# Kernel optimization log

Measured on AMD Instinct MI355X. Metric: run time of the kernel, lower is better.

## Reference

```python
import jax, jax.numpy as jnp
import numpy as np

B, S, H = 2, 2048, 2048
NH = 16
NOPE, ROPE, VDIM, RANK = 128, 64, 128, 512
QHD = NOPE + ROPE  # 192
MAX_POS, THETA = 4096, 50000.0
EPS = 1e-6


def rms_norm(x, w):
    var = jnp.mean(x.astype(jnp.float32) ** 2, axis=-1, keepdims=True)
    return (x * jax.lax.rsqrt(var + EPS)).astype(x.dtype) * w


def deinterleave(x):
    # view(..., d//2, 2).transpose(-1,-2).reshape(..., d): [x0,x2,...,x1,x3,...]
    return jnp.concatenate([x[..., ::2], x[..., 1::2]], axis=-1)


def rotate_half(x):
    x1, x2 = jnp.split(x, 2, axis=-1)
    return jnp.concatenate([-x2, x1], axis=-1)


def setup_inputs() -> dict:
    key = jax.random.key(0)
    ks = jax.random.split(key, 6)
    hidden_states = jax.random.normal(ks[0], (B, S, H), dtype=jnp.float32)
    attention_mask = jnp.broadcast_to(jnp.tril(jnp.ones((S, S), dtype=bool))[None, None], (B, 1, S, S))
    position_ids = jnp.broadcast_to(jnp.arange(S, dtype=jnp.int32)[None], (B, S))
    inv_freq = 1.0 / (THETA ** (jnp.arange(0, ROPE, 2, dtype=jnp.float32) / ROPE))
    freqs = jnp.arange(MAX_POS, dtype=jnp.float32)[:, None] * inv_freq[None, :]
    emb = jnp.concatenate([freqs, freqs], axis=-1)
    cos_cache, sin_cache = jnp.cos(emb), jnp.sin(emb)
    Wq = jax.random.normal(ks[1], (H, NH * QHD), dtype=jnp.float32) * 0.02
    Wkv_a = jax.random.normal(ks[2], (H, RANK + ROPE), dtype=jnp.float32) * 0.02
    kv_a_ln_w = jnp.ones((RANK,), dtype=jnp.float32)
    Wkv_b = jax.random.normal(ks[3], (NH, NOPE + VDIM, RANK), dtype=jnp.float32) * 0.02
    Wo = jax.random.normal(ks[4], (NH * VDIM, H), dtype=jnp.float32) * 0.02
    return {"hidden_states": hidden_states, "attention_mask": attention_mask, "position_ids": position_ids,
            "cos_cache": cos_cache, "sin_cache": sin_cache, "Wq": Wq, "Wkv_a": Wkv_a,
            "kv_a_ln_w": kv_a_ln_w, "Wkv_b": Wkv_b, "Wo": Wo}


def reference(hidden_states, attention_mask, position_ids, cos_cache, sin_cache, Wq, Wkv_a, kv_a_ln_w, Wkv_b, Wo):
    bsz, q_len, _ = hidden_states.shape
    scale = QHD ** (-0.5)
    # Q projection: [b,s,h*192] -> [b,h,s,192]
    q = (hidden_states @ Wq).reshape(bsz, q_len, NH, QHD).transpose(0, 2, 1, 3)
    q_nope, q_pe = q[..., :NOPE], q[..., NOPE:]
    # compressed KV + shared rope key: [b,s,576]
    ckv_full = hidden_states @ Wkv_a
    compressed_kv, k_pe = ckv_full[..., :RANK], ckv_full[..., RANK:]
    compressed_kv = rms_norm(compressed_kv, kv_a_ln_w)  # [b,s,512]
    # interleaved -> half layout, then standard RoPE
    q_pe = deinterleave(q_pe)                     # [b,h,s,64]
    k_pe = deinterleave(k_pe)                     # [b,s,64]
    cos = cos_cache[position_ids][:, None]        # [b,1,s,64]
    sin = sin_cache[position_ids][:, None]
    q_pe = q_pe * cos + rotate_half(q_pe) * sin
    k_pe = (k_pe[:, None] * cos + rotate_half(k_pe[:, None]) * sin)[:, 0]  # [b,s,64]
    # weight absorption
    q_absorb = Wkv_b[:, :NOPE]    # [h,128,512]
    out_absorb = Wkv_b[:, NOPE:]  # [h,128,512]
    q_nope_c = jnp.einsum('hdc,bhqd->bhqc', q_absorb, q_nope)  # [b,h,s,512]
    scores = (jnp.einsum('bhqd,bkd->bhqk', q_pe, k_pe)
              + jnp.einsum('bhqc,bkc->bhqk', q_nope_c, compressed_kv)) * scale
    scores = jnp.where(attention_mask, scores, jnp.float32(-1e9))
    probs = jax.nn.softmax(scores.astype(jnp.float32), axis=-1).astype(hidden_states.dtype)
    x = jnp.einsum('bhqk,bkc->bhqc', probs, compressed_kv)     # [b,h,s,512]
    attn = jnp.einsum('bhqc,hdc->bhqd', x, out_absorb)         # [b,h,s,128]
    attn = attn.transpose(0, 2, 1, 3).reshape(bsz, q_len, NH * VDIM)
    return attn @ Wo
```

## Files before the change

### kernel.cpp

```cpp
#include <hip/hip_runtime.h>
#include <math.h>

#define B_    2
#define S_    2048
#define H_    2048
#define NH_   16
#define NOPE_ 128
#define ROPE_ 64
#define VDIM_ 128
#define RANK_ 512
#define QHD_  192
#define DTOT_ 576

typedef short short8 __attribute__((ext_vector_type(8)));
typedef float f32x4 __attribute__((ext_vector_type(4)));

__device__ __forceinline__ unsigned short f2bf(float f) {
    unsigned u = __float_as_uint(f);
    u += 0x7fffu + ((u >> 16) & 1u);
    return (unsigned short)(u >> 16);
}
__device__ __forceinline__ float bf2f(unsigned short u) {
    return __uint_as_float((unsigned)u << 16);
}
__device__ __forceinline__ unsigned pack2bf(float a, float b) {
    return (unsigned)f2bf(a) | ((unsigned)f2bf(b) << 16);
}
__device__ __forceinline__ unsigned long long pack4bf(float a, float b, float c, float d) {
    return (unsigned long long)pack2bf(a, b) | ((unsigned long long)pack2bf(c, d) << 32);
}
union i4s8 { int4 i; short8 s; };

typedef __attribute__((address_space(3))) unsigned int lds_u32_t;
typedef __attribute__((address_space(1))) const unsigned int glob_u32_t;
__device__ __forceinline__ void async_copy16(const unsigned short* g, unsigned short* l) {
    __builtin_amdgcn_global_load_lds((glob_u32_t*)g, (lds_u32_t*)l, 16, 0, 0);
}

__global__ __launch_bounds__(256) void cast_bf16(const float* __restrict__ in,
                                                 unsigned short* __restrict__ out)
{
    const size_t i = ((size_t)blockIdx.x * 256 + threadIdx.x) * 4;
    float4 v = *(const float4*)(in + i);
    *(unsigned long long*)(out + i) = pack4bf(v.x, v.y, v.z, v.w);
}

__global__ __launch_bounds__(256) void transpose_w(const float* __restrict__ in,
                                                   unsigned short* __restrict__ out,
                                                   int Rr, int Cc,
                                                   size_t inBatch, size_t outBatch)
{
    __shared__ unsigned short tl[64][72];
    in  += (size_t)blockIdx.z * inBatch;
    out += (size_t)blockIdx.z * outBatch;
    const int t  = threadIdx.x;
    const int r0 = blockIdx.x * 64;
    const int c0 = blockIdx.y * 64;
    const int lr = t >> 4;
    const int lc = (t & 15) * 4;
#pragma unroll
    for (int r = 0; r < 4; ++r) {
        float4 v = *(const float4*)(in + (size_t)(r0 + lr*4 + r) * Cc + c0 + lc);
        tl[lr*4 + r][lc+0] = f2bf(v.x); tl[lr*4 + r][lc+1] = f2bf(v.y);
        tl[lr*4 + r][lc+2] = f2bf(v.z); tl[lr*4 + r][lc+3] = f2bf(v.w);
    }
    __syncthreads();
#pragma unroll
    for (int r = 0; r < 4; ++r) {
        ushort4 v;
        v.x = tl[lc+0][lr*4+r]; v.y = tl[lc+1][lr*4+r];
        v.z = tl[lc+2][lr*4+r]; v.w = tl[lc+3][lr*4+r];
        *(ushort4*)(out + (size_t)(c0 + lr*4 + r) * Rr + r0 + lc) = v;
    }
}

#define BGEMM_BODY(STORE_STMT)                                                     \
    __shared__ unsigned short Al[128*32];                                          \
    __shared__ unsigned short Bl[128*32];                                          \
    const int t = threadIdx.x;                                                     \
    const int wv = t >> 6;                                                         \
    const int lane = t & 63;                                                       \
    const int lq = lane & 15, quad = lane >> 4;                                    \
    const int m0 = by * 128, n0 = bx * 128;                                        \
    const int wrow = (wv >> 1) * 64, wcol = (wv & 1) * 64;                         \
    const int srow = lane >> 2;                                                    \
    const int scol = (lane & 3) * 8;                                               \
    f32x4 acc[4][4] = {};                                                          \
    for (int k0 = 0; k0 < K; k0 += 32) {                                           \
        _Pragma("unroll")                                                          \
        for (int pA = 0; pA < 2; ++pA) {                                           \
            const unsigned short* src =                                            \
                A + (size_t)(m0 + pA*64 + wv*16 + srow) * lda + k0 + scol;         \
            async_copy16(src, &Al[pA*2048 + wv*512]);                              \
        }                                                                          \
        _Pragma("unroll")                                                          \
        for (int pB = 0; pB < 2; ++pB) {                                           \
            int brow = n0 + pB*64 + wv*16 + srow;                                  \
            if (brow > N - 1) brow = N - 1;                                        \
            const unsigned short* src = B + (size_t)brow * ldb + k0 + scol;        \
            async_copy16(src, &Bl[pB*2048 + wv*512]);                              \
        }                                                                          \
        __syncthreads();                                                           \
        short8 af[4], bf[4];                                                       \
        _Pragma("unroll")                                                          \
        for (int i = 0; i < 4; ++i) {                                              \
            af[i] = *(const short8*)&Al[(wrow + i*16 + lq)*32 + quad*8];           \
            bf[i] = *(const short8*)&Bl[(wcol + i*16 + lq)*32 + quad*8];           \
        }                                                                          \
        _Pragma("unroll")                                                          \
        for (int mi = 0; mi < 4; ++mi)                                             \
            _Pragma("unroll")                                                      \
            for (int ni = 0; ni < 4; ++ni)                                         \
                acc[mi][ni] = __builtin_amdgcn_mfma_f32_16x16x32_bf16(             \
                    af[mi], bf[ni], acc[mi][ni], 0, 0, 0);                         \
        __syncthreads();                                                           \
    }                                                                              \
    _Pragma("unroll")                                                              \
    for (int mi = 0; mi < 4; ++mi)                                                 \
        _Pragma("unroll")                                                          \
        for (int ni = 0; ni < 4; ++ni) {                                           \
            int col = n0 + wcol + ni*16 + lq;                                      \
            if (col < N) {                                                         \
                _Pragma("unroll")                                                  \
                for (int r = 0; r < 4; ++r)                                        \
                    STORE_STMT;                                                    \
            }                                                                      \
        }

#define XCD_SWZ(BX, BY)                                                            \
    {                                                                              \
        const int nx = gridDim.x;                                                  \
        const int nwg = nx * gridDim.y;                                            \
        const int wg = BY * nx + BX;                                               \
        const int nw = (wg & 7) * (nwg >> 3) + (wg >> 3);                          \
        BX = nw % nx; BY = nw / nx;                                                \
    }

__global__ __launch_bounds__(256, 2) void bgemm2(const unsigned short* __restrict__ A,
                                                 int lda,
                                                 const unsigned short* __restrict__ B,
                                                 int ldb,
                                                 unsigned short* __restrict__ C,
                                                 int ldc, int K, int N, int qcmode)
{
    int bx = blockIdx.x, by = blockIdx.y;
    if (qcmode == 1) {
        const int z = blockIdx.z;
        A += (size_t)(z >> 4) * S_ * (NH_*QHD_) + (z & 15) * QHD_;
        B += (size_t)(z & 15) * RANK_ * NOPE_;
        C += (size_t)z * S_ * DTOT_;
    } else if (qcmode == 2) {
        const int z = blockIdx.z;
        A += (size_t)(z & 15) * 256 * RANK_ + (size_t)NOPE_ * RANK_;
        B += (size_t)(z >> 4) * S_ * DTOT_;
        C += (size_t)z * VDIM_ * S_;
    } else {
        XCD_SWZ(bx, by);
    }
    BGEMM_BODY(C[(size_t)(m0 + wrow + mi*16 + quad*4 + r) * ldc + col] = f2bf(acc[mi][ni][r]))
}

__global__ __launch_bounds__(256, 2) void bgemm2f(const unsigned short* __restrict__ A,
                                                  int lda,
                                                  const unsigned short* __restrict__ B,
                                                  int ldb,
                                                  float* __restrict__ C,
                                                  int ldc, int K, int N)
{
    int bx = blockIdx.x, by = blockIdx.y;
    XCD_SWZ(bx, by);
    BGEMM_BODY(C[(size_t)(m0 + wrow + mi*16 + quad*4 + r) * ldc + col] = acc[mi][ni][r])
}

__global__ __launch_bounds__(128) void postkv(const unsigned short* __restrict__ ckv_bf,
                                              const float* __restrict__ lnw,
                                              const int*   __restrict__ pos_ids,
                                              const float* __restrict__ cosc,
                                              const float* __restrict__ sinc,
                                              unsigned short* __restrict__ k_cat)
{
    const int row = blockIdx.x;
    const int t   = threadIdx.x;
    const unsigned short* src = ckv_bf + (size_t)row * DTOT_;
    __shared__ float red[128];

    ushort4 v = *(const ushort4*)(src + t * 4);
    float x0 = bf2f(v.x), x1 = bf2f(v.y), x2 = bf2f(v.z), x3 = bf2f(v.w);
    red[t] = x0*x0 + x1*x1 + x2*x2 + x3*x3;
    __syncthreads();
    for (int off = 64; off > 0; off >>= 1) {
        if (t < off) red[t] += red[t + off];
        __syncthreads();
    }
    const float rs = rsqrtf(red[0] / (float)RANK_ + 1e-6f);

    unsigned short* kc = k_cat + (size_t)row * DTOT_;
    *(unsigned long long*)(kc + t*4) =
        pack4bf(x0*rs*lnw[t*4+0], x1*rs*lnw[t*4+1], x2*rs*lnw[t*4+2], x3*rs*lnw[t*4+3]);

    if (t < 32) {
        const int pos = pos_ids[row];
        const float c  = cosc[pos * ROPE_ + t];
        const float sn = sinc[pos * ROPE_ + t];
        const float y0 = bf2f(src[RANK_ + 2*t]);
        const float y1 = bf2f(src[RANK_ + 2*t + 1]);
        kc[RANK_ + t]      = f2bf(y0*c - y1*sn);
        kc[RANK_ + 32 + t] = f2bf(y1*c + y0*sn);
    }
}

__global__ __launch_bounds__(512) void ropeq(const unsigned short* __restrict__ q_bf,
                                             const int*   __restrict__ pos_ids,
                                             const float* __restrict__ cosc,
                                             const float* __restrict__ sinc,
                                             unsigned short* __restrict__ q_cat)
{
    const int row = blockIdx.x;
    const int t   = threadIdx.x;
    const int h   = t >> 5;
    const int i   = t & 31;
    const int pos = pos_ids[row];
    const float c  = cosc[pos * ROPE_ + i];
    const float sn = sinc[pos * ROPE_ + i];
    const unsigned short* qrow = q_bf + (size_t)row * (NH_*QHD_) + h * QHD_ + NOPE_;
    const float x0 = bf2f(qrow[2*i]);
    const float x1 = bf2f(qrow[2*i + 1]);
    const int b = row >> 11, s = row & 2047;
    unsigned short* qc = q_cat + ((size_t)(b * NH_ + h) * S_ + s) * DTOT_ + RANK_;
    qc[i]      = f2bf(x0*c - x1*sn);
    qc[32 + i] = f2bf(x1*c + x0*sn);
}

__global__ __launch_bounds__(256) void wcast(const float* __restrict__ w,
                                             unsigned short* __restrict__ wbf)
{
    const size_t i = ((size_t)blockIdx.x * 256 + threadIdx.x) * 4;
    float4 v = *(const float4*)(w + i);
    *(unsigned long long*)(wbf + i) = pack4bf(v.x, v.y, v.z, v.w);
}

__device__ __forceinline__ short8 quad_transpose(unsigned d0, unsigned d1,
                                                 unsigned d2, unsigned d3,
                                                 int srcA, int srcB, bool lowquad)
{
    int e0 = __shfl((int)d0, srcA, 64);
    int e1 = __shfl((int)d1, srcA, 64);
    int e2 = __shfl((int)d2, srcA, 64);
    int e3 = __shfl((int)d3, srcA, 64);
    int f0 = __shfl((int)d0, srcB, 64);
    int f1 = __shfl((int)d1, srcB, 64);
    int f2 = __shfl((int)d2, srcB, 64);
    int f3 = __shfl((int)d3, srcB, 64);
    i4s8 u;
    u.i.x = lowquad ? e0 : e2;
    u.i.y = lowquad ? e1 : e3;
    u.i.z = lowquad ? f0 : f2;
    u.i.w = lowquad ? f1 : f3;
    return u.s;
}

__global__ __launch_bounds__(256, 2) void flash_attn4(
    const unsigned short* __restrict__ q_cat,
    const unsigned short* __restrict__ k_cat,
    const unsigned short* __restrict__ vwt,
    unsigned short* __restrict__ attn_bf)
{
    __shared__ unsigned short sKa[32*512];
    __shared__ unsigned short sKb[32*64];
    __shared__ unsigned short sVW[128*32];

    const int t    = threadIdx.x;
    const int wv   = t >> 6;
    const int lane = t & 63;
    const int lq   = lane & 15;
    const int quad = lane >> 4;
    const int h    = blockIdx.x;
    const int q0   = (31 - blockIdx.y) * 64;
    const int b    = blockIdx.z;
    const int srcA = lq + ((quad & 1) << 5);
    const int srcB = srcA + 16;
    const bool lowq = quad < 2;
    const int myq  = q0 + wv*16 + lq;

    const unsigned short* qrow =
        q_cat + (((size_t)(b*NH_ + h)) * S_ + q0 + wv*16 + lq) * DTOT_ + quad*8;
    short8 qf[18];
#pragma unroll
    for (int c = 0; c < 18; ++c) qf[c] = *(const short8*)(qrow + c*32);

    const unsigned short* kcb = k_cat + (size_t)b * S_ * DTOT_;
    const unsigned short* vtb = vwt + (size_t)(b*NH_ + h) * VDIM_ * S_;

    f32x4 o[8];
#pragma unroll
    for (int i = 0; i < 8; ++i) o[i] = (f32x4){0.f, 0.f, 0.f, 0.f};
    float m_i = -1e30f, l_i = 0.f;
    const float scale = 0.0721687836f;
    const int ntiles = (q0 >> 5) + 2;

    const int swz  = lq & 7;
    const int selA = (swz >> 2) * 32;
    const int selB = 32 - selA;
    const int kqo  = (quad ^ (swz & 3)) * 8;
    const unsigned short* kr0a = &sKa[lq*512 + kqo];
    const unsigned short* kr1a = &sKa[(16 + lq)*512 + kqo];
    const unsigned short* kr0b = &sKb[lq*64 + kqo];
    const unsigned short* kr1b = &sKb[(16 + lq)*64 + kqo];

    const int kq0 = wv*DTOT_ + (lane ^ wv)*8;
    const int kq1 = wv*DTOT_ + (lane ^ (wv + 4))*8;
    const int kob = (t >> 3)*DTOT_ + RANK_ + ((t & 7) ^ ((t >> 3) & 7))*8;

    const int vrow  = wv*16 + (lane >> 2);
    const int vgcol = (((lane & 3) ^ ((lane >> 3) & 3))) * 8;
    const int pvsw  = (quad ^ ((lq >> 1) & 3)) * 8;

#define ISSUE_K(TPTR)                                                          \
    _Pragma("unroll")                                                          \
    for (int p = 0; p < 8; ++p)                                                \
        async_copy16((TPTR) + (p*4)*DTOT_ + ((p & 1) ? kq1 : kq0),             \
                     &sKa[p*2048 + wv*512]);                                   \
    async_copy16((TPTR) + kob, &sKb[wv*512])

    const unsigned short* ktp = kcb;
    ISSUE_K(ktp);
    ktp += 32 * DTOT_;

    for (int tt = 0; tt < ntiles; ++tt) {
        const int k0 = tt << 5;
        __syncthreads();
        {
#pragma unroll
            for (int p = 0; p < 2; ++p) {
                const unsigned short* vsrc =
                    vtb + (size_t)(p*64 + vrow) * S_ + k0 + vgcol;
                async_copy16(vsrc, &sVW[p*2048 + wv*512]);
            }
        }
        f32x4 s0a = {0.f,0.f,0.f,0.f}, s0b = {0.f,0.f,0.f,0.f};
        f32x4 s1a = {0.f,0.f,0.f,0.f}, s1b = {0.f,0.f,0.f,0.f};
        __builtin_amdgcn_s_setprio(1);
#pragma unroll
        for (int c = 0; c < 16; c += 2) {
            short8 ka0 = *(const short8*)(kr0a + c*32 + selA);
            short8 kb0 = *(const short8*)(kr0a + c*32 + selB);
            short8 ka1 = *(const short8*)(kr1a + c*32 + selA);
            short8 kb1 = *(const short8*)(kr1a + c*32 + selB);
            s0a = __builtin_amdgcn_mfma_f32_16x16x32_bf16(ka0, qf[c],   s0a, 0, 0, 0);
            s1a = __builtin_amdgcn_mfma_f32_16x16x32_bf16(ka1, qf[c],   s1a, 0, 0, 0);
            s0b = __builtin_amdgcn_mfma_f32_16x16x32_bf16(kb0, qf[c+1], s0b, 0, 0, 0);
            s1b = __builtin_amdgcn_mfma_f32_16x16x32_bf16(kb1, qf[c+1], s1b, 0, 0, 0);
        }
        {
            short8 ka0 = *(const short8*)(kr0b + selA);
            short8 kb0 = *(const short8*)(kr0b + selB);
            short8 ka1 = *(const short8*)(kr1b + selA);
            short8 kb1 = *(const short8*)(kr1b + selB);
            s0a = __builtin_amdgcn_mfma_f32_16x16x32_bf16(ka0, qf[16], s0a, 0, 0, 0);
            s1a = __builtin_amdgcn_mfma_f32_16x16x32_bf16(ka1, qf[16], s1a, 0, 0, 0);
            s0b = __builtin_amdgcn_mfma_f32_16x16x32_bf16(kb0, qf[17], s0b, 0, 0, 0);
            s1b = __builtin_amdgcn_mfma_f32_16x16x32_bf16(kb1, qf[17], s1b, 0, 0, 0);
        }
        __builtin_amdgcn_s_setprio(0);
        float sv[8];
#pragma unroll
        for (int r = 0; r < 4; ++r) {
            int kk0 = k0 + quad*4 + r;
            sv[r]     = (kk0      <= myq) ? (s0a[r] + s0b[r]) * scale : -1e30f;
            sv[r + 4] = (kk0 + 16 <= myq) ? (s1a[r] + s1b[r]) * scale : -1e30f;
        }
        float mx = sv[0];
#pragma unroll
        for (int i = 1; i < 8; ++i) mx = fmaxf(mx, sv[i]);
        mx = fmaxf(mx, __shfl_xor(mx, 16));
        mx = fmaxf(mx, __shfl_xor(mx, 32));
        if (!__all(mx <= m_i + 8.f)) {
            const float m_new = fmaxf(m_i, mx);
            const float alpha = __expf(m_i - m_new);
            m_i = m_new;
            l_i *= alpha;
#pragma unroll
            for (int i = 0; i < 8; ++i) {
                o[i][0]*=alpha; o[i][1]*=alpha; o[i][2]*=alpha; o[i][3]*=alpha;
            }
        }
        float p[8]; float ls = 0.f;
#pragma unroll
        for (int i = 0; i < 8; ++i) { p[i] = __expf(sv[i] - m_i); ls += p[i]; }
        ls += __shfl_xor(ls, 16);
        ls += __shfl_xor(ls, 32);
        l_i += ls;
        short8 pb = quad_transpose(pack2bf(p[0], p[1]), pack2bf(p[2], p[3]),
                                   pack2bf(p[4], p[5]), pack2bf(p[6], p[7]),
                                   srcA, srcB, lowq);
        __syncthreads();
        if (tt + 1 < ntiles) {
            ISSUE_K(ktp);
            ktp += 32 * DTOT_;
        }
        __builtin_amdgcn_s_setprio(1);
#pragma unroll
        for (int dt = 0; dt < 8; ++dt) {
            short8 va = *(const short8*)&sVW[(dt*16 + lq)*32 + pvsw];
            o[dt] = __builtin_amdgcn_mfma_f32_16x16x32_bf16(va, pb, o[dt], 0, 0, 0);
        }
        __builtin_amdgcn_s_setprio(0);
    }

    const float inv = 1.0f / l_i;
    unsigned short* orow =
        attn_bf + ((size_t)b * S_ + q0 + wv*16 + lq) * (NH_*VDIM_) + h*VDIM_;
#pragma unroll
    for (int dt2 = 0; dt2 < 4; ++dt2) {
        short8 xa = quad_transpose(
            pack2bf(o[2*dt2][0]*inv,   o[2*dt2][1]*inv),
            pack2bf(o[2*dt2][2]*inv,   o[2*dt2][3]*inv),
            pack2bf(o[2*dt2+1][0]*inv, o[2*dt2+1][1]*inv),
            pack2bf(o[2*dt2+1][2]*inv, o[2*dt2+1][3]*inv),
            srcA, srcB, lowq);
        *(short8*)(orow + dt2*32 + quad*8) = xa;
    }
}

extern "C" void kernel_launch(void* const* d_in, const int* in_sizes, int n_in,
                              void* d_out, int out_size, void* d_ws, size_t ws_size,
                              hipStream_t stream)
{
    const float* hidden  = (const float*)d_in[0];
    const int*   pos_ids = (const int*)d_in[2];
    const float* cosc    = (const float*)d_in[3];
    const float* sinc    = (const float*)d_in[4];
    const float* Wq      = (const float*)d_in[5];
    const float* Wkv_a   = (const float*)d_in[6];
    const float* lnw     = (const float*)d_in[7];
    const float* Wkv_b   = (const float*)d_in[8];
    const float* Wo      = (const float*)d_in[9];
    float* out = (float*)d_out;

    const int M = B_ * S_;
    char* ws = (char*)d_ws;
    unsigned short* hidden_bf = (unsigned short*)ws;
    unsigned short* vwT       = (unsigned short*)ws;
    unsigned short* q_bf      = (unsigned short*)(ws + 16777216);
    unsigned short* attn_bf   = q_bf;
    unsigned short* ckv_bf    = (unsigned short*)(ws + 41943040);
    unsigned short* wqaT      = ckv_bf;
    unsigned short* q_cat     = (unsigned short*)(ws + 46661632);
    unsigned short* k_cat     = (unsigned short*)(ws + 122159104);
    unsigned short* wT        = (unsigned short*)(ws + 126877696);
    unsigned short* w2bf      = (unsigned short*)(ws + 126877696 + 8388608);

    cast_bf16<<<8192, 256, 0, stream>>>(hidden, hidden_bf);
    transpose_w<<<dim3(32, 48, 1), 256, 0, stream>>>(Wq, wT, H_, NH_*QHD_, 0, 0);
    bgemm2<<<dim3(24, 32, 1), 256, 0, stream>>>(hidden_bf, H_, wT, H_, q_bf, NH_*QHD_, H_, NH_*QHD_, 0);
    transpose_w<<<dim3(32, 9, 1), 256, 0, stream>>>(Wkv_a, wT, H_, DTOT_, 0, 0);
    bgemm2<<<dim3(5, 32, 1), 256, 0, stream>>>(hidden_bf, H_, wT, H_, ckv_bf, DTOT_, H_, DTOT_, 0);
    postkv<<<M, 128, 0, stream>>>(ckv_bf, lnw, pos_ids, cosc, sinc, k_cat);
    ropeq<<<M, 512, 0, stream>>>(q_bf, pos_ids, cosc, sinc, q_cat);
    wcast<<<(NH_*256*RANK_)/1024, 256, 0, stream>>>(Wkv_b, w2bf);
    bgemm2<<<dim3(16, 1, 32), 256, 0, stream>>>(w2bf, RANK_, k_cat, DTOT_, vwT, S_, RANK_, S_, 2);
    transpose_w<<<dim3(2, 8, 16), 256, 0, stream>>>(Wkv_b, wqaT, NOPE_, RANK_,
                                                    (size_t)256*RANK_, (size_t)RANK_*NOPE_);
    bgemm2<<<dim3(4, 16, 32), 256, 0, stream>>>(q_bf, NH_*QHD_, wqaT, NOPE_, q_cat, DTOT_, NOPE_, RANK_, 1);
    flash_attn4<<<dim3(NH_, S_/64, B_), 256, 0, stream>>>(q_cat, k_cat, vwT, attn_bf);
    transpose_w<<<dim3(32, 32, 1), 256, 0, stream>>>(Wo, wT, H_, H_, 0, 0);
    bgemm2f<<<dim3(16, 32, 1), 256, 0, stream>>>(attn_bf, H_, wT, H_, out, H_, H_, H_);
}
```

Before: 520.4 us.

## Use 256x256 double-buffered async-copy GEMM for Q and output projections

```diff
diff --git a/kernel.cpp b/kernel.cpp
--- a/kernel.cpp
+++ b/kernel.cpp
@@ -73,6 +73,15 @@
         *(ushort4*)(out + (size_t)(c0 + lr*4 + r) * Rr + r0 + lc) = v;
     }
 }
+
+#define XCD_SWZ(BX, BY)                                                            \
+    {                                                                              \
+        const int nx = gridDim.x;                                                  \
+        const int nwg = nx * gridDim.y;                                            \
+        const int wg = BY * nx + BX;                                               \
+        const int nw = (wg & 7) * (nwg >> 3) + (wg >> 3);                          \
+        BX = nw % nx; BY = nw / nx;                                                \
+    }
 
 #define BGEMM_BODY(STORE_STMT)                                                     \
     __shared__ unsigned short Al[128*32];                                          \
@@ -127,15 +136,6 @@
             }                                                                      \
         }
 
-#define XCD_SWZ(BX, BY)                                                            \
-    {                                                                              \
-        const int nx = gridDim.x;                                                  \
-        const int nwg = nx * gridDim.y;                                            \
-        const int wg = BY * nx + BX;                                               \
-        const int nw = (wg & 7) * (nwg >> 3) + (wg >> 3);                          \
-        BX = nw % nx; BY = nw / nx;                                                \
-    }
-
 __global__ __launch_bounds__(256, 2) void bgemm2(const unsigned short* __restrict__ A,
                                                  int lda,
                                                  const unsigned short* __restrict__ B,
@@ -160,16 +160,153 @@
     BGEMM_BODY(C[(size_t)(m0 + wrow + mi*16 + quad*4 + r) * ldc + col] = f2bf(acc[mi][ni][r]))
 }
 
-__global__ __launch_bounds__(256, 2) void bgemm2f(const unsigned short* __restrict__ A,
+#define PHASE_BAR() { __builtin_amdgcn_sched_barrier(0);                           \
+    asm volatile("" ::: "memory");                                                 \
+    __builtin_amdgcn_s_barrier();                                                  \
+    asm volatile("" ::: "memory");                                                 \
+    __builtin_amdgcn_sched_barrier(0); }
+
+#define STG_A(Q, TT) {                                                             \
+    const unsigned short* s_ = A + (size_t)(m0 + (Q)*128) * lda + (TT)*64 + stA;   \
+    async_copy16(s_,                  &sA[((TT)&1)*16384 + (Q)*8192 + wid*512]);   \
+    async_copy16(s_ + (size_t)64*lda, &sA[((TT)&1)*16384 + (Q)*8192 + 4096 + wid*512]); }
+#define STG_B(Q, TT) {                                                             \
+    const unsigned short* s_ = B + (size_t)(n0 + (Q)*128) * ldb + (TT)*64 + stB;   \
+    async_copy16(s_,                  &sB[((TT)&1)*16384 + (Q)*8192 + wid*512]);   \
+    async_copy16(s_ + (size_t)64*ldb, &sB[((TT)&1)*16384 + (Q)*8192 + 4096 + wid*512]); }
+
+#define G256_BODY(STORE_STMT)                                                      \
+    __shared__ unsigned short sA[2*16384];                                         \
+    __shared__ unsigned short sB[2*16384];                                         \
+    const int t    = threadIdx.x;                                                  \
+    const int wid  = t >> 6;                                                       \
+    const int lane = t & 63;                                                       \
+    const int lq = lane & 15, quad = lane >> 4;                                    \
+    const int wm = wid >> 2, wn = wid & 3;                                         \
+    int bx = blockIdx.x, by = blockIdx.y;                                          \
+    XCD_SWZ(bx, by);                                                               \
+    const int m0 = by * 256, n0 = bx * 256;                                        \
+    const int nt = K >> 6;                                                         \
+    const int trow = t >> 3;                                                       \
+    const int gcol = ((t & 7) ^ (trow & 7)) * 8;                                   \
+    const size_t stA = (size_t)trow * lda + gcol;                                  \
+    const size_t stB = (size_t)trow * ldb + gcol;                                  \
+    const int swz  = lq & 7;                                                       \
+    const int selA = (swz >> 2) * 32;                                              \
+    const int selB2 = 32 - selA;                                                   \
+    const int kqo  = (quad ^ (swz & 3)) * 8;                                       \
+    const int aoff = (wm*128 + lq)*64 + kqo;                                       \
+    const int boff = (wn*64  + lq)*64 + kqo;                                       \
+    f32x4 acc[8][4] = {};                                                          \
+                       \
+    STG_B(0, 0); STG_A(0, 0); STG_A(1, 0); STG_B(1, 0);                            \
+    STG_B(0, 1); STG_A(0, 1);                                                      \
+    asm volatile("s_waitcnt vmcnt(4)" ::: "memory");                               \
+    PHASE_BAR();                                                                   \
+    for (int u = 0; u < nt; ++u) {                                                 \
+        const unsigned short* aB = &sA[(u & 1)*16384 + aoff];                      \
+        const unsigned short* bB = &sB[(u & 1)*16384 + boff];                      \
+        short8 a03[4][2], a47[4][2], b01[2][2], b23[2][2];                         \
+                                                                \
+        _Pragma("unroll")                                                          \
+        for (int rf = 0; rf < 4; ++rf) {                                           \
+            a03[rf][0] = *(const short8*)(aB + rf*1024 + selA);                    \
+            a03[rf][1] = *(const short8*)(aB + rf*1024 + selB2);                   \
+        }                                                                          \
+        _Pragma("unroll")                                                          \
+        for (int nf = 0; nf < 2; ++nf) {                                           \
+            b01[nf][0] = *(const short8*)(bB + nf*1024 + selA);                    \
+            b01[nf][1] = *(const short8*)(bB + nf*1024 + selB2);                   \
+        }                                                                          \
+        if (u + 1 < nt) { STG_A(1, u + 1); }                                       \
+        _Pragma("unroll")                                                          \
+        for (int rf = 0; rf < 4; ++rf)                                             \
+            _Pragma("unroll")                                                      \
+            for (int nf = 0; nf < 2; ++nf) {                                       \
+                acc[rf][nf] = __builtin_amdgcn_mfma_f32_16x16x32_bf16(             \
+                    a03[rf][0], b01[nf][0], acc[rf][nf], 0, 0, 0);                 \
+                acc[rf][nf] = __builtin_amdgcn_mfma_f32_16x16x32_bf16(             \
+                    a03[rf][1], b01[nf][1], acc[rf][nf], 0, 0, 0);                 \
+            }                                                                      \
+        PHASE_BAR();                                                               \
+                                                                \
+        _Pragma("unroll")                                                          \
+        for (int nf = 0; nf < 2; ++nf) {                                           \
+            b23[nf][0] = *(const short8*)(bB + (2 + nf)*1024 + selA);              \
+            b23[nf][1] = *(const short8*)(bB + (2 + nf)*1024 + selB2);             \
+        }                                                                          \
+        if (u + 1 < nt) { STG_B(1, u + 1); }                                       \
+        _Pragma("unroll")                                                          \
+        for (int rf = 0; rf < 4; ++rf)                                             \
+            _Pragma("unroll")                                                      \
+            for (int nf = 0; nf < 2; ++nf) {                                       \
+                acc[rf][2 + nf] = __builtin_amdgcn_mfma_f32_16x16x32_bf16(         \
+                    a03[rf][0], b23[nf][0], acc[rf][2 + nf], 0, 0, 0);             \
+                acc[rf][2 + nf] = __builtin_amdgcn_mfma_f32_16x16x32_bf16(         \
+                    a03[rf][1], b23[nf][1], acc[rf][2 + nf], 0, 0, 0);             \
+            }                                                                      \
+        PHASE_BAR();                                                               \
+                                                                \
+        _Pragma("unroll")                                                          \
+        for (int rf = 0; rf < 4; ++rf) {                                           \
+            a47[rf][0] = *(const short8*)(aB + (4 + rf)*1024 + selA);              \
+            a47[rf][1] = *(const short8*)(aB + (4 + rf)*1024 + selB2);             \
+        }                                                                          \
+        if (u + 2 < nt) { STG_B(0, u + 2); }                                       \
+        _Pragma("unroll")                                                          \
+        for (int rf = 0; rf < 4; ++rf)                                             \
+            _Pragma("unroll")                                                      \
+            for (int nf = 0; nf < 2; ++nf) {                                       \
+                acc[4 + rf][nf] = __builtin_amdgcn_mfma_f32_16x16x32_bf16(         \
+                    a47[rf][0], b01[nf][0], acc[4 + rf][nf], 0, 0, 0);             \
+                acc[4 + rf][nf] = __builtin_amdgcn_mfma_f32_16x16x32_bf16(         \
+                    a47[rf][1], b01[nf][1], acc[4 + rf][nf], 0, 0, 0);             \
+            }                                                                      \
+        PHASE_BAR();                                                               \
+                                                                \
+        if (u + 2 < nt) { STG_A(0, u + 2); }                                       \
+        _Pragma("unroll")                                                          \
+        for (int rf = 0; rf < 4; ++rf)                                             \
+            _Pragma("unroll")                                                      \
+            for (int nf = 0; nf < 2; ++nf) {                                       \
+                acc[4 + rf][2 + nf] = __builtin_amdgcn_mfma_f32_16x16x32_bf16(     \
+                    a47[rf][0], b23[nf][0], acc[4 + rf][2 + nf], 0, 0, 0);         \
+                acc[4 + rf][2 + nf] = __builtin_amdgcn_mfma_f32_16x16x32_bf16(     \
+                    a47[rf][1], b23[nf][1], acc[4 + rf][2 + nf], 0, 0, 0);         \
+            }                                                                      \
+        if (u + 2 < nt) { asm volatile("s_waitcnt vmcnt(4)" ::: "memory"); }       \
+        else            { asm volatile("s_waitcnt vmcnt(0)" ::: "memory"); }       \
+        PHASE_BAR();                                                               \
+    }                                                                              \
+    _Pragma("unroll")                                                              \
+    for (int rf = 0; rf < 8; ++rf)                                                 \
+        _Pragma("unroll")                                                          \
+        for (int nf = 0; nf < 4; ++nf) {                                           \
+            const size_t rb = (size_t)(m0 + wm*128 + rf*16 + quad*4) * ldc         \
+                              + n0 + wn*64 + nf*16 + lq;                           \
+            _Pragma("unroll")                                                      \
+            for (int r = 0; r < 4; ++r)                                            \
+                STORE_STMT;                                                        \
+        }
+
+__global__ __launch_bounds__(512, 2) void gemm256(const unsigned short* __restrict__ A,
                                                   int lda,
                                                   const unsigned short* __restrict__ B,
                                                   int ldb,
-                                                  float* __restrict__ C,
-                                                  int ldc, int K, int N)
-{
-    int bx = blockIdx.x, by = blockIdx.y;
-    XCD_SWZ(bx, by);
-    BGEMM_BODY(C[(size_t)(m0 + wrow + mi*16 + quad*4 + r) * ldc + col] = acc[mi][ni][r])
+                                                  unsigned short* __restrict__ C,
+                                                  int ldc, int K)
+{
+    G256_BODY(C[rb + (size_t)r*ldc] = f2bf(acc[rf][nf][r]))
+}
+
+__global__ __launch_bounds__(512, 2) void gemm256f(const unsigned short* __restrict__ A,
+                                                   int lda,
+                                                   const unsigned short* __restrict__ B,
+                                                   int ldb,
+                                                   float* __restrict__ C,
+                                                   int ldc, int K)
+{
+    G256_BODY(C[rb + (size_t)r*ldc] = acc[rf][nf][r])
 }
 
 __global__ __launch_bounds__(128) void postkv(const unsigned short* __restrict__ ckv_bf,
@@ -339,7 +476,6 @@
         }
         f32x4 s0a = {0.f,0.f,0.f,0.f}, s0b = {0.f,0.f,0.f,0.f};
         f32x4 s1a = {0.f,0.f,0.f,0.f}, s1b = {0.f,0.f,0.f,0.f};
-        __builtin_amdgcn_s_setprio(1);
 #pragma unroll
         for (int c = 0; c < 16; c += 2) {
             short8 ka0 = *(const short8*)(kr0a + c*32 + selA);
@@ -361,7 +497,6 @@
             s0b = __builtin_amdgcn_mfma_f32_16x16x32_bf16(kb0, qf[17], s0b, 0, 0, 0);
             s1b = __builtin_amdgcn_mfma_f32_16x16x32_bf16(kb1, qf[17], s1b, 0, 0, 0);
         }
-        __builtin_amdgcn_s_setprio(0);
         float sv[8];
 #pragma unroll
         for (int r = 0; r < 4; ++r) {
@@ -398,13 +533,11 @@
             ISSUE_K(ktp);
             ktp += 32 * DTOT_;
         }
-        __builtin_amdgcn_s_setprio(1);
 #pragma unroll
         for (int dt = 0; dt < 8; ++dt) {
             short8 va = *(const short8*)&sVW[(dt*16 + lq)*32 + pvsw];
             o[dt] = __builtin_amdgcn_mfma_f32_16x16x32_bf16(va, pb, o[dt], 0, 0, 0);
         }
-        __builtin_amdgcn_s_setprio(0);
     }
 
     const float inv = 1.0f / l_i;
@@ -452,7 +585,7 @@
 
     cast_bf16<<<8192, 256, 0, stream>>>(hidden, hidden_bf);
     transpose_w<<<dim3(32, 48, 1), 256, 0, stream>>>(Wq, wT, H_, NH_*QHD_, 0, 0);
-    bgemm2<<<dim3(24, 32, 1), 256, 0, stream>>>(hidden_bf, H_, wT, H_, q_bf, NH_*QHD_, H_, NH_*QHD_, 0);
+    gemm256<<<dim3(12, 16), 512, 0, stream>>>(hidden_bf, H_, wT, H_, q_bf, NH_*QHD_, H_);
     transpose_w<<<dim3(32, 9, 1), 256, 0, stream>>>(Wkv_a, wT, H_, DTOT_, 0, 0);
     bgemm2<<<dim3(5, 32, 1), 256, 0, stream>>>(hidden_bf, H_, wT, H_, ckv_bf, DTOT_, H_, DTOT_, 0);
     postkv<<<M, 128, 0, stream>>>(ckv_bf, lnw, pos_ids, cosc, sinc, k_cat);
@@ -464,5 +597,5 @@
     bgemm2<<<dim3(4, 16, 32), 256, 0, stream>>>(q_bf, NH_*QHD_, wqaT, NOPE_, q_cat, DTOT_, NOPE_, RANK_, 1);
     flash_attn4<<<dim3(NH_, S_/64, B_), 256, 0, stream>>>(q_cat, k_cat, vwT, attn_bf);
     transpose_w<<<dim3(32, 32, 1), 256, 0, stream>>>(Wo, wT, H_, H_, 0, 0);
-    bgemm2f<<<dim3(16, 32, 1), 256, 0, stream>>>(attn_bf, H_, wT, H_, out, H_, H_, H_);
-}
+    gemm256f<<<dim3(8, 16), 512, 0, stream>>>(attn_bf, H_, wT, H_, out, H_, H_);
+}
```

After: 518.9 us. Within noise of the previous version (-0.3%).
